# Optimization experiments

Measured on AMD Instinct MI355X. Metric: run time of the kernel, lower is better.

Reference implementation:

```python
import jax, jax.numpy as jnp
import numpy as np

B, S, D, H = 2, 2048, 1024, 16
DK = D // H


def setup_inputs() -> dict:
    key = jax.random.key(0)
    ks = jax.random.split(key, 7)
    x = jax.random.normal(ks[0], (B, S, D), dtype=jnp.float32)
    gamma = jax.random.normal(ks[1], (D,), dtype=jnp.float32)
    mask = jax.random.randint(ks[2], (B, S), 0, 2, dtype=jnp.int32)
    w_qkv_w = jax.random.normal(ks[3], (D, 3 * D), dtype=jnp.float32) / np.sqrt(D)
    w_qkv_b = jax.random.normal(ks[4], (3 * D,), dtype=jnp.float32) * 0.02
    w_o_w = jax.random.normal(ks[5], (D, D), dtype=jnp.float32) / np.sqrt(D)
    w_o_b = jax.random.normal(ks[6], (D,), dtype=jnp.float32) * 0.02
    return {"x": x, "gamma": gamma, "mask": mask, "w_qkv_w": w_qkv_w,
            "w_qkv_b": w_qkv_b, "w_o_w": w_o_w, "w_o_b": w_o_b}


def reference(x, gamma, mask, w_qkv_w, w_qkv_b, w_o_w, w_o_b):
    b, s, d = x.shape
    # QKV projection, then per-head interleaved chunk (matches torch view+chunk)
    qkv = x @ w_qkv_w + w_qkv_b                      # [B,S,3D]
    qkv = qkv.reshape(b, s, H, 3 * DK).transpose(0, 2, 1, 3)  # [B,H,S,3*dk]
    q, k, v = jnp.split(qkv, 3, axis=-1)             # each [B,H,S,dk]
    scale = 1.0 / np.sqrt(DK).astype(np.float32)
    scores = jnp.einsum('bhqd,bhkd->bhqk', q, k) * scale  # [B,H,S,S]
    m = mask[:, None, None, :]                       # 2D mask -> [B,1,1,S]
    scores = jnp.where(m == 0, -jnp.inf, scores)
    attn = jax.nn.softmax(scores, axis=-1)           # dropout p=0.0 -> identity
    out = jnp.einsum('bhqk,bhkd->bhqd', attn, v)     # [B,H,S,dk]
    out = out.transpose(0, 2, 1, 3).reshape(b, s, d) # [B,S,D]
    out = out @ w_o_w + w_o_b
    return (gamma + 1.0) * out
```

## Files before the change

kernel.cpp:

```cpp
#include <hip/hip_runtime.h>
#include <hip/hip_bf16.h>


using bf16 = __hip_bfloat16;
typedef __attribute__((ext_vector_type(8))) short bf16x8;
typedef __attribute__((ext_vector_type(4))) short bf16x4;
typedef __attribute__((ext_vector_type(4))) float f32x4;

#define QSCALE 0.18033688011112042f

static __device__ __forceinline__ f32x4 mfma_bf16(bf16x8 a, bf16x8 b, f32x4 c) {
    return __builtin_amdgcn_mfma_f32_16x16x32_bf16(a, b, c, 0, 0, 0);
}

static __device__ __forceinline__ void gld_lds16(const void* g, void* s) {
    __builtin_amdgcn_global_load_lds(
        (const __attribute__((address_space(1))) unsigned int*)g,
        (__attribute__((address_space(3))) unsigned int*)s,
        16, 0, 0);
}

static __device__ __forceinline__ short f2s(float f) {
    bf16 h = __float2bfloat16(f);
    return *reinterpret_cast<short*>(&h);
}

__global__ void cast_bf16_kernel(const float* __restrict__ in, bf16* __restrict__ out, int n4) {
    int i = blockIdx.x * blockDim.x + threadIdx.x;
    if (i >= n4) return;
    float4 f = reinterpret_cast<const float4*>(in)[i];
    out[4*i+0] = __float2bfloat16(f.x);
    out[4*i+1] = __float2bfloat16(f.y);
    out[4*i+2] = __float2bfloat16(f.z);
    out[4*i+3] = __float2bfloat16(f.w);
}

__global__ void transpose_cast_kernel(const float* __restrict__ in, bf16* __restrict__ out,
                                      int R, int C) {
    __shared__ float tile[32][33];
    int c0 = blockIdx.x * 32, r0 = blockIdx.y * 32;
    int x = threadIdx.x, y = threadIdx.y;
#pragma unroll
    for (int i = 0; i < 32; i += 8) tile[y + i][x] = in[(size_t)(r0 + y + i) * C + c0 + x];
    __syncthreads();
#pragma unroll
    for (int i = 0; i < 32; i += 8)
        out[(size_t)(c0 + y + i) * R + r0 + x] = __float2bfloat16(tile[x][y + i]);
}

__global__ void transpose_v_kernel(const bf16* __restrict__ in, bf16* __restrict__ out) {
    __shared__ bf16 t[64][72];
    const int bh = blockIdx.y, s0 = blockIdx.x * 64;
    const int r = threadIdx.x >> 2, c16 = (threadIdx.x & 3) * 16;
    const uint4* src = (const uint4*)(in + ((size_t)bh * 2048 + s0 + r) * 64 + c16);
    uint4 a = src[0], b = src[1];
    *(uint4*)&t[r][c16] = a;
    *(uint4*)&t[r][c16 + 8] = b;
    __syncthreads();
    bf16 tmp[16];
#pragma unroll
    for (int i = 0; i < 16; ++i) tmp[i] = t[c16 + i][r];
    uint4* dst = (uint4*)(out + ((size_t)bh * 64 + r) * 2048 + s0 + c16);
    dst[0] = ((uint4*)tmp)[0];
    dst[1] = ((uint4*)tmp)[1];
}

template <int EPI, int TM, int MINW>
__global__ __launch_bounds__(256, MINW)
void gemm_bt_kernel(const bf16* __restrict__ A, const bf16* __restrict__ Bt,
                    int M, int N, int K,
                    const float* __restrict__ bias, const float* __restrict__ gamma,
                    bf16* __restrict__ Qout, bf16* __restrict__ Kout, bf16* __restrict__ Vout,
                    float* __restrict__ Cout) {
    constexpr int MI = TM / 32;
    constexpr int CA = TM / 32;
    __shared__ __align__(16) bf16 As[TM * 64];
    __shared__ __align__(16) bf16 Bs[128 * 64];

    const int tid  = threadIdx.x;
    const int wave = tid >> 6, lane = tid & 63;
    const int quad = lane >> 4, l16 = lane & 15;
    const int wr = wave >> 1, wc = wave & 1;
    const int bm = blockIdx.y, bn = blockIdx.x;

    f32x4 acc[MI][4] = {};

    const int crow = lane >> 3;
    const int sblk = (lane & 7) ^ (crow & 7);
    const bf16* gA[CA]; const bf16* gB[4]; bf16* lA[CA]; bf16* lB[4];
#pragma unroll
    for (int c = 0; c < CA; ++c) {
        int ch = wave * CA + c;
        gA[c] = A + (size_t)(bm * TM + ch * 8 + crow) * K + sblk * 8;
        lA[c] = As + ch * 512 + lane * 8;
    }
#pragma unroll
    for (int c = 0; c < 4; ++c) {
        int ch = wave * 4 + c;
        gB[c] = Bt + (size_t)(bn * 128 + ch * 8 + crow) * K + sblk * 8;
        lB[c] = Bs + ch * 512 + lane * 8;
    }
    const int xr = l16 & 7;

    for (int k0 = 0; k0 < K; k0 += 64) {
#pragma unroll
        for (int c = 0; c < CA; ++c) gld_lds16(gA[c] + k0, lA[c]);
#pragma unroll
        for (int c = 0; c < 4; ++c) gld_lds16(gB[c] + k0, lB[c]);
        __syncthreads();
#pragma unroll
        for (int ks = 0; ks < 2; ++ks) {
            bf16x8 af[MI], bfr[4];
#pragma unroll
            for (int mi = 0; mi < MI; ++mi)
                af[mi] = *(const bf16x8*)(As + (wr * (TM/2) + mi * 16 + l16) * 64 + ((4 * ks + quad) ^ xr) * 8);
#pragma unroll
            for (int ni = 0; ni < 4; ++ni)
                bfr[ni] = *(const bf16x8*)(Bs + (wc * 64 + ni * 16 + l16) * 64 + ((4 * ks + quad) ^ xr) * 8);
#pragma unroll
            for (int mi = 0; mi < MI; ++mi)
#pragma unroll
                for (int ni = 0; ni < 4; ++ni)
                    acc[mi][ni] = mfma_bf16(af[mi], bfr[ni], acc[mi][ni]);
        }
        __syncthreads();
    }

#pragma unroll
    for (int mi = 0; mi < MI; ++mi) {
#pragma unroll
        for (int ni = 0; ni < 4; ++ni) {
#pragma unroll
            for (int r = 0; r < 4; ++r) {
                int row = bm * TM + wr * (TM/2) + mi * 16 + quad * 4 + r;
                int col = bn * 128 + wc * 64 + ni * 16 + l16;
                float v = acc[mi][ni][r];
                if (EPI == 0) {
                    v += bias[col];
                    int h = col / 192;
                    int rr = col - h * 192;
                    int which = rr >> 6, dk = rr & 63;
                    int b = row >> 11, s = row & 2047;
                    size_t bh = (size_t)b * 16 + h;
                    if (which == 0) {
                        Qout[(bh * 2048 + s) * 64 + dk] = __float2bfloat16(v * QSCALE);
                    } else if (which == 1) {
                        Kout[(bh * 2048 + s) * 64 + dk] = __float2bfloat16(v);
                    } else {
                        Vout[(bh * 2048 + s) * 64 + dk] = __float2bfloat16(v);
                    }
                } else {
                    float o = (gamma[col] + 1.0f) * (v + bias[col]);
                    Cout[(size_t)row * N + col] = o;
                }
            }
        }
    }
}

__global__ __launch_bounds__(256, 2)
void attn_kernel(const bf16* __restrict__ Qb, const bf16* __restrict__ Kb,
                 const bf16* __restrict__ Vt, const int* __restrict__ mask,
                 bf16* __restrict__ Aout) {
    __shared__ __align__(16) bf16 Ks[2][64 * 72];
    __shared__ __align__(16) bf16 Vs[2][64 * 76];
    __shared__ __align__(16) float Biass[2][64];

    const int bh = blockIdx.y;
    const int b = bh >> 4, h = bh & 15;
    const int q0 = blockIdx.x * 128;
    const int tid = threadIdx.x;
    const int wave = tid >> 6, lane = tid & 63;
    const int quad = lane >> 4, l16 = lane & 15;

    bf16x8 aq[2][2];
#pragma unroll
    for (int m = 0; m < 2; ++m) {
        const bf16* qp = Qb + ((size_t)bh * 2048 + q0 + wave * 32 + m * 16 + l16) * 64;
        aq[m][0] = *(const bf16x8*)(qp + quad * 8);
        aq[m][1] = *(const bf16x8*)(qp + 32 + quad * 8);
    }

    bf16x8 ones;
#pragma unroll
    for (int j = 0; j < 8; ++j) ones[j] = (short)0x3F80;

    f32x4 O[2][4] = {};
    f32x4 Lacc[2] = {};

    const int srow = tid >> 2, spart = tid & 3;
    const bf16* gK = Kb + ((size_t)bh * 2048 + srow) * 64 + spart * 16;
    const bf16* gV = Vt + ((size_t)bh * 64 + srow) * 2048 + spart * 16;
    uint4* lK[2]; uint4* lV[2];
#pragma unroll
    for (int p = 0; p < 2; ++p) {
        lK[p] = (uint4*)(Ks[p] + srow * 72 + spart * 16);
        lV[p] = (uint4*)(Vs[p] + srow * 76 + spart * 16);
    }

    uint4 kr0, kr1, vr0, vr1; int mreg = 1;
    {
        const uint4* nk = (const uint4*)gK;
        const uint4* nv = (const uint4*)gV;
        kr0 = nk[0]; kr1 = nk[1]; vr0 = nv[0]; vr1 = nv[1];
        if (tid < 64) mreg = mask[b * 2048 + tid];
        lK[0][0] = kr0; lK[0][1] = kr1;
        lV[0][0] = vr0; lV[0][1] = vr1;
        if (tid < 64) Biass[0][tid] = mreg ? -24.0f : -1e30f;
        const uint4* nk1 = (const uint4*)(gK + 4096);
        const uint4* nv1 = (const uint4*)(gV + 64);
        kr0 = nk1[0]; kr1 = nk1[1]; vr0 = nv1[0]; vr1 = nv1[1];
        if (tid < 64) mreg = mask[b * 2048 + 64 + tid];
    }

    for (int kt = 0; kt < 32; ++kt) {
        __syncthreads();
        const int cur = kt & 1, nxt = cur ^ 1;

        if (kt + 1 < 32) {
            lK[nxt][0] = kr0; lK[nxt][1] = kr1;
            lV[nxt][0] = vr0; lV[nxt][1] = vr1;
            if (tid < 64) Biass[nxt][tid] = mreg ? -24.0f : -1e30f;
        }
        if (kt + 2 < 32) {
            const uint4* nk = (const uint4*)(gK + (size_t)(kt + 2) * 4096);
            const uint4* nv = (const uint4*)(gV + (kt + 2) * 64);
            kr0 = nk[0]; kr1 = nk[1]; vr0 = nv[0]; vr1 = nv[1];
            if (tid < 64) mreg = mask[b * 2048 + (kt + 2) * 64 + tid];
        }

        f32x4 bias4[4];
        bf16x8 bk[4][2];
#pragma unroll
        for (int kt4 = 0; kt4 < 4; ++kt4) {
            bias4[kt4] = *(const f32x4*)(&Biass[cur][0] + kt4 * 16 + quad * 4);
            const bf16* kp = Ks[cur] + (kt4 * 16 + l16) * 72 + quad * 8;
            bk[kt4][0] = *(const bf16x8*)kp;
            bk[kt4][1] = *(const bf16x8*)(kp + 32);
        }
        bf16x8 bv8[2][4];
#pragma unroll
        for (int a = 0; a < 2; ++a) {
#pragma unroll
            for (int nt = 0; nt < 4; ++nt) {
                const bf16* vp = Vs[cur] + (nt * 16 + l16) * 76 + a * 32 + quad * 4;
                bf16x4 lo = *(const bf16x4*)vp;
                bf16x4 hi = *(const bf16x4*)(vp + 16);
                bf16x8 f;
                f[0] = lo[0]; f[1] = lo[1]; f[2] = lo[2]; f[3] = lo[3];
                f[4] = hi[0]; f[5] = hi[1]; f[6] = hi[2]; f[7] = hi[3];
                bv8[a][nt] = f;
            }
        }

#pragma unroll
        for (int m = 0; m < 2; ++m) {
            f32x4 sv[4];
#pragma unroll
            for (int kt4 = 0; kt4 < 4; ++kt4) {
                f32x4 c = {0.f, 0.f, 0.f, 0.f};
                c = mfma_bf16(bk[kt4][0], aq[m][0], c);
                c = mfma_bf16(bk[kt4][1], aq[m][1], c);
                sv[kt4] = c;
            }
            float p[4][4];
#pragma unroll
            for (int kt4 = 0; kt4 < 4; ++kt4)
#pragma unroll
                for (int r = 0; r < 4; ++r)
                    p[kt4][r] = __builtin_amdgcn_exp2f(sv[kt4][r] + bias4[kt4][r]);

#pragma unroll
            for (int a = 0; a < 2; ++a) {
                bf16x8 pa;
                pa[0] = f2s(p[2*a][0]);   pa[1] = f2s(p[2*a][1]);
                pa[2] = f2s(p[2*a][2]);   pa[3] = f2s(p[2*a][3]);
                pa[4] = f2s(p[2*a+1][0]); pa[5] = f2s(p[2*a+1][1]);
                pa[6] = f2s(p[2*a+1][2]); pa[7] = f2s(p[2*a+1][3]);
                Lacc[m] = mfma_bf16(pa, ones, Lacc[m]);
#pragma unroll
                for (int nt = 0; nt < 4; ++nt)
                    O[m][nt] = mfma_bf16(pa, bv8[a][nt], O[m][nt]);
            }
        }
    }

#pragma unroll
    for (int m = 0; m < 2; ++m) {
        float inv[4];
#pragma unroll
        for (int r = 0; r < 4; ++r) inv[r] = __builtin_amdgcn_rcpf(Lacc[m][r]);
#pragma unroll
        for (int nt = 0; nt < 4; ++nt) {
#pragma unroll
            for (int r = 0; r < 4; ++r) {
                int row = q0 + wave * 32 + m * 16 + quad * 4 + r;
                Aout[((size_t)b * 2048 + row) * 1024 + h * 64 + nt * 16 + l16] =
                    __float2bfloat16(O[m][nt][r] * inv[r]);
            }
        }
    }
}

extern "C" void kernel_launch(void* const* d_in, const int* in_sizes, int n_in,
                              void* d_out, int out_size, void* d_ws, size_t ws_size,
                              hipStream_t stream) {
    const float* x     = (const float*)d_in[0];
    const float* gamma = (const float*)d_in[1];
    const int*   mask  = (const int*)d_in[2];
    const float* wqkv  = (const float*)d_in[3];
    const float* bqkv  = (const float*)d_in[4];
    const float* wo    = (const float*)d_in[5];
    const float* bo    = (const float*)d_in[6];
    float* out = (float*)d_out;

    char* ws = (char*)d_ws;
    const size_t MB = 1u << 20;
    bf16* xb    = (bf16*)(ws);
    bf16* wqkvT = (bf16*)(ws + 8 * MB);
    bf16* woT   = (bf16*)(ws + 14 * MB);
    bf16* Qb    = (bf16*)(ws + 16 * MB);
    bf16* Kb    = (bf16*)(ws + 24 * MB);
    bf16* Vt    = (bf16*)(ws + 32 * MB);
    bf16* Vtmp  = (bf16*)(ws + 40 * MB);
    bf16* attn  = (bf16*)(ws + 40 * MB);

    cast_bf16_kernel<<<4096, 256, 0, stream>>>(x, xb, 4194304 / 4);
    transpose_cast_kernel<<<dim3(96, 32), dim3(32, 8), 0, stream>>>(wqkv, wqkvT, 1024, 3072);
    transpose_cast_kernel<<<dim3(32, 32), dim3(32, 8), 0, stream>>>(wo, woT, 1024, 1024);

    gemm_bt_kernel<0, 128, 3><<<dim3(24, 32), 256, 0, stream>>>(
        xb, wqkvT, 4096, 3072, 1024, bqkv, nullptr, Qb, Kb, Vtmp, nullptr);

    transpose_v_kernel<<<dim3(32, 32), 256, 0, stream>>>(Vtmp, Vt);

    attn_kernel<<<dim3(16, 32), 256, 0, stream>>>(Qb, Kb, Vt, mask, attn);

    gemm_bt_kernel<1, 64, 4><<<dim3(8, 64), 256, 0, stream>>>(
        attn, woT, 4096, 1024, 1024, bo, gamma, nullptr, nullptr, nullptr, out);
}
```

Baseline: 195.0 us.

## Merge prep kernels and rework attention with direct-to-LDS loads and swizzle

The three cast/transpose kernels become one prep launch, which cuts launch overhead. The attention kernel now uses 2 waves of 128 threads, each handling 64 query rows, and loads K/V tiles with global_load_lds into XOR-swizzled unpadded LDS instead of staging them through registers. The V transpose permutes columns so the attention kernel can read V fragments with single 16-byte loads instead of two 8-byte loads. In exchange, each wave holds more accumulator registers and there are fewer waves per block, which may reduce latency hiding, and the swizzle and permutation logic has to stay in sync.

```diff
diff --git a/kernel.cpp b/kernel.cpp
--- a/kernel.cpp
+++ b/kernel.cpp
@@ -4,7 +4,6 @@
 
 using bf16 = __hip_bfloat16;
 typedef __attribute__((ext_vector_type(8))) short bf16x8;
-typedef __attribute__((ext_vector_type(4))) short bf16x4;
 typedef __attribute__((ext_vector_type(4))) float f32x4;
 
 #define QSCALE 0.18033688011112042f
@@ -25,27 +24,36 @@
     return *reinterpret_cast<short*>(&h);
 }
 
-__global__ void cast_bf16_kernel(const float* __restrict__ in, bf16* __restrict__ out, int n4) {
-    int i = blockIdx.x * blockDim.x + threadIdx.x;
-    if (i >= n4) return;
-    float4 f = reinterpret_cast<const float4*>(in)[i];
-    out[4*i+0] = __float2bfloat16(f.x);
-    out[4*i+1] = __float2bfloat16(f.y);
-    out[4*i+2] = __float2bfloat16(f.z);
-    out[4*i+3] = __float2bfloat16(f.w);
-}
-
-__global__ void transpose_cast_kernel(const float* __restrict__ in, bf16* __restrict__ out,
-                                      int R, int C) {
+__global__ void prep_kernel(const float* __restrict__ x, bf16* __restrict__ xb,
+                            const float* __restrict__ wqkv, bf16* __restrict__ wqkvT,
+                            const float* __restrict__ wo, bf16* __restrict__ woT) {
     __shared__ float tile[32][33];
-    int c0 = blockIdx.x * 32, r0 = blockIdx.y * 32;
-    int x = threadIdx.x, y = threadIdx.y;
-#pragma unroll
-    for (int i = 0; i < 32; i += 8) tile[y + i][x] = in[(size_t)(r0 + y + i) * C + c0 + x];
+    int blk = blockIdx.x;
+    if (blk < 4096) {
+        int i = blk * 256 + threadIdx.x;
+        float4 f = reinterpret_cast<const float4*>(x)[i];
+        xb[4*i+0] = __float2bfloat16(f.x);
+        xb[4*i+1] = __float2bfloat16(f.y);
+        xb[4*i+2] = __float2bfloat16(f.z);
+        xb[4*i+3] = __float2bfloat16(f.w);
+        return;
+    }
+    const float* in; bf16* out; int R, C, bx, by;
+    if (blk < 7168) {
+        int idx = blk - 4096; in = wqkv; out = wqkvT; R = 1024; C = 3072;
+        bx = idx % 96; by = idx / 96;
+    } else {
+        int idx = blk - 7168; in = wo; out = woT; R = 1024; C = 1024;
+        bx = idx & 31; by = idx >> 5;
+    }
+    int c0 = bx * 32, r0 = by * 32;
+    int xo = threadIdx.x & 31, yo = threadIdx.x >> 5;
+#pragma unroll
+    for (int i = 0; i < 32; i += 8) tile[yo + i][xo] = in[(size_t)(r0 + yo + i) * C + c0 + xo];
     __syncthreads();
 #pragma unroll
     for (int i = 0; i < 32; i += 8)
-        out[(size_t)(c0 + y + i) * R + r0 + x] = __float2bfloat16(tile[x][y + i]);
+        out[(size_t)(c0 + yo + i) * R + r0 + xo] = __float2bfloat16(tile[xo][yo + i]);
 }
 
 __global__ void transpose_v_kernel(const bf16* __restrict__ in, bf16* __restrict__ out) {
@@ -53,13 +61,18 @@
     const int bh = blockIdx.y, s0 = blockIdx.x * 64;
     const int r = threadIdx.x >> 2, c16 = (threadIdx.x & 3) * 16;
     const uint4* src = (const uint4*)(in + ((size_t)bh * 2048 + s0 + r) * 64 + c16);
-    uint4 a = src[0], b = src[1];
-    *(uint4*)&t[r][c16] = a;
-    *(uint4*)&t[r][c16 + 8] = b;
+    uint4 a0 = src[0], a1 = src[1];
+    *(uint4*)&t[r][c16] = a0;
+    *(uint4*)&t[r][c16 + 8] = a1;
     __syncthreads();
     bf16 tmp[16];
 #pragma unroll
-    for (int i = 0; i < 16; ++i) tmp[i] = t[c16 + i][r];
+    for (int ii = 0; ii < 16; ++ii) {
+        int i = c16 + ii;
+        int a = i >> 5, rem = i & 31, q = rem >> 3, jj = rem & 7;
+        int sp = a * 32 + q * 4 + (jj < 4 ? jj : 16 + jj - 4);
+        tmp[ii] = t[sp][r];
+    }
     uint4* dst = (uint4*)(out + ((size_t)bh * 64 + r) * 2048 + s0 + c16);
     dst[0] = ((uint4*)tmp)[0];
     dst[1] = ((uint4*)tmp)[1];
@@ -158,13 +171,13 @@
     }
 }
 
-__global__ __launch_bounds__(256, 2)
+__global__ __launch_bounds__(128, 1)
 void attn_kernel(const bf16* __restrict__ Qb, const bf16* __restrict__ Kb,
-                 const bf16* __restrict__ Vt, const int* __restrict__ mask,
+                 const bf16* __restrict__ Vtp, const int* __restrict__ mask,
                  bf16* __restrict__ Aout) {
-    __shared__ __align__(16) bf16 Ks[2][64 * 72];
-    __shared__ __align__(16) bf16 Vs[2][64 * 76];
-    __shared__ __align__(16) float Biass[2][64];
+    __shared__ __align__(16) bf16 Ks[2][64 * 64];
+    __shared__ __align__(16) bf16 Vs[2][64 * 64];
+    __shared__ float Biass[2][64];
 
     const int bh = blockIdx.y;
     const int b = bh >> 4, h = bh & 15;
@@ -172,11 +185,12 @@
     const int tid = threadIdx.x;
     const int wave = tid >> 6, lane = tid & 63;
     const int quad = lane >> 4, l16 = lane & 15;
-
-    bf16x8 aq[2][2];
-#pragma unroll
-    for (int m = 0; m < 2; ++m) {
-        const bf16* qp = Qb + ((size_t)bh * 2048 + q0 + wave * 32 + m * 16 + l16) * 64;
+    const int xr = l16 & 7;
+
+    bf16x8 aq[4][2];
+#pragma unroll
+    for (int m = 0; m < 4; ++m) {
+        const bf16* qp = Qb + ((size_t)bh * 2048 + q0 + wave * 64 + m * 16 + l16) * 64;
         aq[m][0] = *(const bf16x8*)(qp + quad * 8);
         aq[m][1] = *(const bf16x8*)(qp + 32 + quad * 8);
     }
@@ -185,32 +199,31 @@
 #pragma unroll
     for (int j = 0; j < 8; ++j) ones[j] = (short)0x3F80;
 
-    f32x4 O[2][4] = {};
-    f32x4 Lacc[2] = {};
-
-    const int srow = tid >> 2, spart = tid & 3;
-    const bf16* gK = Kb + ((size_t)bh * 2048 + srow) * 64 + spart * 16;
-    const bf16* gV = Vt + ((size_t)bh * 64 + srow) * 2048 + spart * 16;
-    uint4* lK[2]; uint4* lV[2];
-#pragma unroll
-    for (int p = 0; p < 2; ++p) {
-        lK[p] = (uint4*)(Ks[p] + srow * 72 + spart * 16);
-        lV[p] = (uint4*)(Vs[p] + srow * 76 + spart * 16);
-    }
-
-    uint4 kr0, kr1, vr0, vr1; int mreg = 1;
-    {
-        const uint4* nk = (const uint4*)gK;
-        const uint4* nv = (const uint4*)gV;
-        kr0 = nk[0]; kr1 = nk[1]; vr0 = nv[0]; vr1 = nv[1];
-        if (tid < 64) mreg = mask[b * 2048 + tid];
-        lK[0][0] = kr0; lK[0][1] = kr1;
-        lV[0][0] = vr0; lV[0][1] = vr1;
-        if (tid < 64) Biass[0][tid] = mreg ? -24.0f : -1e30f;
-        const uint4* nk1 = (const uint4*)(gK + 4096);
-        const uint4* nv1 = (const uint4*)(gV + 64);
-        kr0 = nk1[0]; kr1 = nk1[1]; vr0 = nv1[0]; vr1 = nv1[1];
-        if (tid < 64) mreg = mask[b * 2048 + 64 + tid];
+    f32x4 O[4][4] = {};
+    f32x4 Lacc[4] = {};
+
+    const int r8 = lane >> 3, b8 = lane & 7;
+    const int srcb = b8 ^ r8;
+    const bf16* gK = Kb  + ((size_t)bh * 2048 + wave * 8 + r8) * 64 + srcb * 8;
+    const bf16* gV = Vtp + ((size_t)bh * 64 + wave * 8 + r8) * 2048 + srcb * 8;
+    bf16* lK[2][4]; bf16* lV[2][4];
+#pragma unroll
+    for (int p = 0; p < 2; ++p)
+#pragma unroll
+        for (int c = 0; c < 4; ++c) {
+            lK[p][c] = Ks[p] + c * 1024 + wave * 512 + lane * 8;
+            lV[p][c] = Vs[p] + c * 1024 + wave * 512 + lane * 8;
+        }
+
+    int mreg = 0;
+#pragma unroll
+    for (int c = 0; c < 4; ++c) {
+        gld_lds16(gK + c * 1024, lK[0][c]);
+        gld_lds16(gV + (size_t)c * 32768, lV[0][c]);
+    }
+    if (tid < 64) {
+        Biass[0][tid] = mask[b * 2048 + tid] ? -24.0f : -1e30f;
+        mreg = mask[b * 2048 + 64 + tid];
     }
 
     for (int kt = 0; kt < 32; ++kt) {
@@ -218,43 +231,33 @@
         const int cur = kt & 1, nxt = cur ^ 1;
 
         if (kt + 1 < 32) {
-            lK[nxt][0] = kr0; lK[nxt][1] = kr1;
-            lV[nxt][0] = vr0; lV[nxt][1] = vr1;
+#pragma unroll
+            for (int c = 0; c < 4; ++c) {
+                gld_lds16(gK + (size_t)(kt + 1) * 4096 + c * 1024, lK[nxt][c]);
+                gld_lds16(gV + (kt + 1) * 64 + (size_t)c * 32768, lV[nxt][c]);
+            }
             if (tid < 64) Biass[nxt][tid] = mreg ? -24.0f : -1e30f;
         }
-        if (kt + 2 < 32) {
-            const uint4* nk = (const uint4*)(gK + (size_t)(kt + 2) * 4096);
-            const uint4* nv = (const uint4*)(gV + (kt + 2) * 64);
-            kr0 = nk[0]; kr1 = nk[1]; vr0 = nv[0]; vr1 = nv[1];
-            if (tid < 64) mreg = mask[b * 2048 + (kt + 2) * 64 + tid];
-        }
+        if (kt + 2 < 32 && tid < 64) mreg = mask[b * 2048 + (kt + 2) * 64 + tid];
 
         f32x4 bias4[4];
         bf16x8 bk[4][2];
 #pragma unroll
         for (int kt4 = 0; kt4 < 4; ++kt4) {
             bias4[kt4] = *(const f32x4*)(&Biass[cur][0] + kt4 * 16 + quad * 4);
-            const bf16* kp = Ks[cur] + (kt4 * 16 + l16) * 72 + quad * 8;
-            bk[kt4][0] = *(const bf16x8*)kp;
-            bk[kt4][1] = *(const bf16x8*)(kp + 32);
+            const bf16* kp = Ks[cur] + (kt4 * 16 + l16) * 64;
+            bk[kt4][0] = *(const bf16x8*)(kp + (quad ^ xr) * 8);
+            bk[kt4][1] = *(const bf16x8*)(kp + ((quad + 4) ^ xr) * 8);
         }
         bf16x8 bv8[2][4];
 #pragma unroll
-        for (int a = 0; a < 2; ++a) {
-#pragma unroll
-            for (int nt = 0; nt < 4; ++nt) {
-                const bf16* vp = Vs[cur] + (nt * 16 + l16) * 76 + a * 32 + quad * 4;
-                bf16x4 lo = *(const bf16x4*)vp;
-                bf16x4 hi = *(const bf16x4*)(vp + 16);
-                bf16x8 f;
-                f[0] = lo[0]; f[1] = lo[1]; f[2] = lo[2]; f[3] = lo[3];
-                f[4] = hi[0]; f[5] = hi[1]; f[6] = hi[2]; f[7] = hi[3];
-                bv8[a][nt] = f;
-            }
-        }
-
-#pragma unroll
-        for (int m = 0; m < 2; ++m) {
+        for (int a = 0; a < 2; ++a)
+#pragma unroll
+            for (int nt = 0; nt < 4; ++nt)
+                bv8[a][nt] = *(const bf16x8*)(Vs[cur] + (nt * 16 + l16) * 64 + ((a * 4 + quad) ^ xr) * 8);
+
+#pragma unroll
+        for (int m = 0; m < 4; ++m) {
             f32x4 sv[4];
 #pragma unroll
             for (int kt4 = 0; kt4 < 4; ++kt4) {
@@ -286,7 +289,7 @@
     }
 
 #pragma unroll
-    for (int m = 0; m < 2; ++m) {
+    for (int m = 0; m < 4; ++m) {
         float inv[4];
 #pragma unroll
         for (int r = 0; r < 4; ++r) inv[r] = __builtin_amdgcn_rcpf(Lacc[m][r]);
@@ -294,7 +297,7 @@
         for (int nt = 0; nt < 4; ++nt) {
 #pragma unroll
             for (int r = 0; r < 4; ++r) {
-                int row = q0 + wave * 32 + m * 16 + quad * 4 + r;
+                int row = q0 + wave * 64 + m * 16 + quad * 4 + r;
                 Aout[((size_t)b * 2048 + row) * 1024 + h * 64 + nt * 16 + l16] =
                     __float2bfloat16(O[m][nt][r] * inv[r]);
             }
@@ -325,16 +328,14 @@
     bf16* Vtmp  = (bf16*)(ws + 40 * MB);
     bf16* attn  = (bf16*)(ws + 40 * MB);
 
-    cast_bf16_kernel<<<4096, 256, 0, stream>>>(x, xb, 4194304 / 4);
-    transpose_cast_kernel<<<dim3(96, 32), dim3(32, 8), 0, stream>>>(wqkv, wqkvT, 1024, 3072);
-    transpose_cast_kernel<<<dim3(32, 32), dim3(32, 8), 0, stream>>>(wo, woT, 1024, 1024);
+    prep_kernel<<<8192, 256, 0, stream>>>(x, xb, wqkv, wqkvT, wo, woT);
 
     gemm_bt_kernel<0, 128, 3><<<dim3(24, 32), 256, 0, stream>>>(
         xb, wqkvT, 4096, 3072, 1024, bqkv, nullptr, Qb, Kb, Vtmp, nullptr);
 
     transpose_v_kernel<<<dim3(32, 32), 256, 0, stream>>>(Vtmp, Vt);
 
-    attn_kernel<<<dim3(16, 32), 256, 0, stream>>>(Qb, Kb, Vt, mask, attn);
+    attn_kernel<<<dim3(16, 32), 128, 0, stream>>>(Qb, Kb, Vt, mask, attn);
 
     gemm_bt_kernel<1, 64, 4><<<dim3(8, 64), 256, 0, stream>>>(
         attn, woT, 4096, 1024, 1024, bo, gamma, nullptr, nullptr, nullptr, out);
```

Measured after the change: 188.8 us. 3.1% less time.
